# Optimization experiments

Hardware: AMD Instinct MI355X
Metric: run time of the kernel (lower is better)

Reference implementation:

```python
import jax, jax.numpy as jnp
import numpy as np

B, L, D = 1, 512, 768
INIT_STD = 0.02


def setup_inputs() -> dict:
    key = jax.random.key(0)
    ks = jax.random.split(key, 6)
    hidden_states = jax.random.normal(ks[0], (B, L, D), dtype=jnp.float32)
    attention_mask = jnp.zeros((B, 1, L), dtype=jnp.float32)  # additive mask
    # nn.Linear weights, stored as [in, out] so forward is x @ W + b
    Wq = jax.random.normal(ks[1], (D, D), dtype=jnp.float32) * INIT_STD
    bq = jnp.zeros((D,), dtype=jnp.float32)
    Wk = jax.random.normal(ks[2], (D, D), dtype=jnp.float32) * INIT_STD
    bk = jnp.zeros((D,), dtype=jnp.float32)
    w_att = jax.random.normal(ks[3], (D,), dtype=jnp.float32) * INIT_STD  # Linear(D,1)
    b_att = jnp.zeros((), dtype=jnp.float32)
    Wt = jax.random.normal(ks[4], (D, D), dtype=jnp.float32) * INIT_STD
    bt = jnp.zeros((D,), dtype=jnp.float32)
    return {
        "hidden_states": hidden_states,
        "attention_mask": attention_mask,
        "Wq": Wq, "bq": bq, "Wk": Wk, "bk": bk,
        "w_att": w_att, "b_att": b_att, "Wt": Wt, "bt": bt,
    }


def reference(hidden_states, attention_mask, Wq, bq, Wk, bk, w_att, b_att, Wt, bt):
    # Additive (Bahdanau) attention
    Q = hidden_states @ Wq + bq                      # [B, L, D]
    K = hidden_states @ Wk + bk                      # [B, L, D]
    # Broadcast add -> tanh -> linear score: the O(B,L,L,D) intermediate
    feats = jnp.tanh(Q[:, :, None, :] + K[:, None, :, :])   # [B, Lq, Lk, D]
    scores = jnp.einsum('bqkd,d->bqk', feats, w_att) + b_att # [B, Lq, Lk]
    scores = scores + attention_mask                 # additive mask, broadcast
    probs = jax.nn.softmax(scores, axis=-1)          # [B, Lq, Lk]
    weighted = jnp.einsum('bqk,bkd->bqd', probs, hidden_states)  # [B, L, D]
    return weighted @ Wt + bt + Q
```

## Files before the change

kernel.cpp:

```cpp
#include <hip/hip_runtime.h>

#define L 512
#define D 768
#define LL (L * L)
#define LOG2E  1.44269504088896341f
#define LOG2E2 2.88539008177792681f
#define DH 8
#define DSEG (D / DH)
#define QB 8

typedef __attribute__((ext_vector_type(8))) short bf16x8;
typedef __attribute__((ext_vector_type(4))) short bf16x4;
typedef __attribute__((ext_vector_type(4))) float f32x4;
typedef __attribute__((ext_vector_type(2))) float f32x2;

__device__ __forceinline__ ushort f2bf(float f) {
    unsigned u = __builtin_bit_cast(unsigned, f);
    u += 0x7FFFu + ((u >> 16) & 1u);
    return (ushort)(u >> 16);
}

__device__ __forceinline__ unsigned cvt_pk(float lo, float hi) {
    unsigned r;
    asm("v_cvt_pk_bf16_f32 %0, %1, %2" : "=v"(r) : "v"(lo), "v"(hi));
    return r;
}

__device__ __forceinline__ f32x2 dup2(float x) { return (f32x2){x, x}; }

template<int MODE>
__global__ __launch_bounds__(256) void gemm_mfma(
    const float* __restrict__ Xf,
    const float* __restrict__ W0, const float* __restrict__ W1,
    const float* __restrict__ W2,
    const ushort* __restrict__ Abf, const ushort* __restrict__ Btbf,
    const float* __restrict__ bq, const float* __restrict__ bk,
    float* __restrict__ Qb, float* __restrict__ Eq,
    float* __restrict__ EkT, ushort* __restrict__ XWtT,
    const float* __restrict__ bt, const float* __restrict__ addend,
    float* __restrict__ out, int K)
{
    const int N = D;
    const int bz = (MODE == 0) ? blockIdx.z : 0;

    constexpr int BSTR = (MODE == 0) ? 76 : 72;
    __shared__ __align__(16) ushort As[32][72];
    __shared__ __align__(16) ushort Bs[64][BSTR];

    const int m0 = blockIdx.y * 32;
    const int n0 = blockIdx.x * 64;
    const int t = threadIdx.x;
    const int l = t & 63, w = t >> 6;
    const int wr = w >> 1, wc = w & 1;
    const int frow = l & 15;
    const int kg = (l >> 4) * 8;

    f32x4 acc[2] = {};

    auto mfma_step = [&]() {
        bf16x8 af[2], bfr[2][2];
        #pragma unroll
        for (int kk = 0; kk < 2; ++kk) {
            af[kk] = *(const bf16x8*)&As[16 * wr + frow][32 * kk + kg];
            #pragma unroll
            for (int fc = 0; fc < 2; ++fc) {
                if constexpr (MODE == 0) {
                    bf16x4 lo = *(const bf16x4*)&Bs[32 * wc + 16 * fc + frow][32 * kk + kg];
                    bf16x4 hi = *(const bf16x4*)&Bs[32 * wc + 16 * fc + frow][32 * kk + kg + 4];
                    bfr[fc][kk] = __builtin_shufflevector(lo, hi, 0, 1, 2, 3, 4, 5, 6, 7);
                } else {
                    bfr[fc][kk] = *(const bf16x8*)&Bs[32 * wc + 16 * fc + frow][32 * kk + kg];
                }
            }
        }
        #pragma unroll
        for (int fc = 0; fc < 2; ++fc) {
            acc[fc] = __builtin_amdgcn_mfma_f32_16x16x32_bf16(af[0], bfr[fc][0], acc[fc], 0, 0, 0);
            acc[fc] = __builtin_amdgcn_mfma_f32_16x16x32_bf16(af[1], bfr[fc][1], acc[fc], 0, 0, 0);
        }
    };

    if constexpr (MODE == 0) {
        const float* Wm = bz == 0 ? W0 : bz == 1 ? W1 : W2;
        const int srow = t >> 3, sk = (t & 7) * 8;
        const int kq = (t >> 4) * 4, nc = (t & 15) * 4;
        const float* ApF = Xf + (m0 + srow) * D + sk;
        const float* WpF = Wm + kq * D + n0 + nc;

        float4 pa0 = *(const float4*)(ApF + 0);
        float4 pa1 = *(const float4*)(ApF + 4);
        float4 pw0 = *(const float4*)(WpF + 0 * D);
        float4 pw1 = *(const float4*)(WpF + 1 * D);
        float4 pw2 = *(const float4*)(WpF + 2 * D);
        float4 pw3 = *(const float4*)(WpF + 3 * D);

        for (int k0 = 0; k0 < K; k0 += 64) {
            if (k0) __syncthreads();
            {
                uint4 av;
                av.x = cvt_pk(pa0.x, pa0.y);
                av.y = cvt_pk(pa0.z, pa0.w);
                av.z = cvt_pk(pa1.x, pa1.y);
                av.w = cvt_pk(pa1.z, pa1.w);
                *(uint4*)&As[srow][sk] = av;
            }
            {
                uint2 b;
                b.x = cvt_pk(pw0.x, pw1.x); b.y = cvt_pk(pw2.x, pw3.x);
                *(uint2*)&Bs[nc + 0][kq] = b;
                b.x = cvt_pk(pw0.y, pw1.y); b.y = cvt_pk(pw2.y, pw3.y);
                *(uint2*)&Bs[nc + 1][kq] = b;
                b.x = cvt_pk(pw0.z, pw1.z); b.y = cvt_pk(pw2.z, pw3.z);
                *(uint2*)&Bs[nc + 2][kq] = b;
                b.x = cvt_pk(pw0.w, pw1.w); b.y = cvt_pk(pw2.w, pw3.w);
                *(uint2*)&Bs[nc + 3][kq] = b;
            }
            __syncthreads();
            if (k0 + 64 < K) {
                pa0 = *(const float4*)(ApF + k0 + 64);
                pa1 = *(const float4*)(ApF + k0 + 68);
                pw0 = *(const float4*)(WpF + (k0 + 64) * D);
                pw1 = *(const float4*)(WpF + (k0 + 65) * D);
                pw2 = *(const float4*)(WpF + (k0 + 66) * D);
                pw3 = *(const float4*)(WpF + (k0 + 67) * D);
            }
            mfma_step();
        }
    } else {
        const int srow = t >> 3, sk = (t & 7) * 8;
        const ushort* Ap  = Abf  + (m0 + srow) * K + sk;
        const ushort* Bp0 = Btbf + (n0 + srow) * K + sk;
        const ushort* Bp1 = Btbf + (n0 + srow + 32) * K + sk;

        uint4 a0 = *(const uint4*)Ap;
        uint4 b0 = *(const uint4*)Bp0;
        uint4 b1 = *(const uint4*)Bp1;

        for (int k0 = 0; k0 < K; k0 += 64) {
            if (k0) __syncthreads();
            *(uint4*)&As[srow][sk]      = a0;
            *(uint4*)&Bs[srow][sk]      = b0;
            *(uint4*)&Bs[srow + 32][sk] = b1;
            __syncthreads();
            if (k0 + 64 < K) {
                a0 = *(const uint4*)(Ap  + k0 + 64);
                b0 = *(const uint4*)(Bp0 + k0 + 64);
                b1 = *(const uint4*)(Bp1 + k0 + 64);
            }
            mfma_step();
        }
    }

    const int rg = (l >> 4) * 4;
    #pragma unroll
    for (int fc = 0; fc < 2; ++fc) {
        const int col = n0 + 32 * wc + 16 * fc + frow;
        const int row0 = m0 + 16 * wr + rg;
        if (MODE == 0 && bz == 2) {
            uint2 e;
            e.x = cvt_pk(acc[fc][0], acc[fc][1]);
            e.y = cvt_pk(acc[fc][2], acc[fc][3]);
            *(uint2*)&XWtT[col * L + row0] = e;
        } else if (MODE == 0 && bz == 1) {
            const float bv = bk[col];
            float4 e;
            e.x = __builtin_amdgcn_exp2f(LOG2E2 * (acc[fc][0] + bv));
            e.y = __builtin_amdgcn_exp2f(LOG2E2 * (acc[fc][1] + bv));
            e.z = __builtin_amdgcn_exp2f(LOG2E2 * (acc[fc][2] + bv));
            e.w = __builtin_amdgcn_exp2f(LOG2E2 * (acc[fc][3] + bv));
            *(float4*)&EkT[col * L + row0] = e;
        } else if (MODE == 0) {
            const float bv = bq[col];
            #pragma unroll
            for (int i = 0; i < 4; ++i) {
                float v = acc[fc][i] + bv;
                Qb[(row0 + i) * N + col] = v;
                Eq[(row0 + i) * N + col] = __builtin_amdgcn_exp2f(LOG2E2 * v);
            }
        } else {
            const float bv = bt[col];
            #pragma unroll
            for (int i = 0; i < 4; ++i)
                out[(row0 + i) * N + col] =
                    acc[fc][i] + bv + addend[(row0 + i) * N + col];
        }
    }
}

__global__ __launch_bounds__(256) void score_k(
    const float* __restrict__ Eq, const float* __restrict__ EkT,
    const float* __restrict__ w_att, float* __restrict__ sP)
{
    __shared__ __align__(16) float eqlds[DSEG][12];
    const int kt = blockIdx.x;
    const int dh = blockIdx.y;
    const int qg = blockIdx.z;
    const int q0 = qg * QB;
    const int dbase = dh * DSEG;
    const int tid = threadIdx.x;
    const int lane = tid & 63, wv = tid >> 6;
    const int k = kt * 256 + wv * 64 + lane;

    {
        const int row = tid >> 5;
        const int j   = tid & 31;
        #pragma unroll
        for (int c = 0; c < 3; ++c) {
            int d = j + 32 * c;
            eqlds[d][row] = Eq[(q0 + row) * D + dbase + d];
        }
        if (tid < 32) {
            #pragma unroll
            for (int c = 0; c < 3; ++c) {
                int d = tid + 32 * c;
                eqlds[d][8] = (-2.f * LOG2E) * w_att[dbase + d];
            }
        }
    }
    __syncthreads();

    const float* __restrict__ ekp = EkT + dbase * L + k;
    const f32x2 one = dup2(1.f);
    f32x2 acc2[4] = {};

    #pragma unroll 2
    for (int d0 = 0; d0 < DSEG; d0 += 4) {
        f32x2 ek0 = dup2(ekp[(d0 + 0) * L]);
        f32x2 ek1 = dup2(ekp[(d0 + 1) * L]);
        f32x2 ek2 = dup2(ekp[(d0 + 2) * L]);
        f32x2 ek3 = dup2(ekp[(d0 + 3) * L]);
        f32x2 w0 = dup2(eqlds[d0 + 0][8]);
        f32x2 w1 = dup2(eqlds[d0 + 1][8]);
        f32x2 w2 = dup2(eqlds[d0 + 2][8]);
        f32x2 w3 = dup2(eqlds[d0 + 3][8]);
        f32x4 Elo[4], Ehi[4];
        #pragma unroll
        for (int dd = 0; dd < 4; ++dd) {
            Elo[dd] = *(const f32x4*)&eqlds[d0 + dd][0];
            Ehi[dd] = *(const f32x4*)&eqlds[d0 + dd][4];
        }
        #pragma unroll
        for (int j = 0; j < 4; ++j) {
            #define GET2(dd) ((j < 2) ? (f32x2){Elo[dd][2 * j], Elo[dd][2 * j + 1]} \
                                      : (f32x2){Ehi[dd][2 * j - 4], Ehi[dd][2 * j - 3]})
            f32x2 e0 = GET2(0);
            f32x2 e1 = GET2(1);
            f32x2 e2 = GET2(2);
            f32x2 e3 = GET2(3);
            #undef GET2
            f32x2 Aa = __builtin_elementwise_fma(e0, ek0, one);
            f32x2 Bb = __builtin_elementwise_fma(e1, ek1, one);
            f32x2 Cc = __builtin_elementwise_fma(e2, ek2, one);
            f32x2 Dd = __builtin_elementwise_fma(e3, ek3, one);
            f32x2 AB = Aa * Bb, CD = Cc * Dd;
            f32x2 N1 = __builtin_elementwise_fma(w0, Bb, w1 * Aa);
            f32x2 N2 = __builtin_elementwise_fma(w2, Dd, w3 * Cc);
            f32x2 Nm = __builtin_elementwise_fma(N1, CD, N2 * AB);
            f32x2 P = AB * CD;
            f32x2 R;
            R.x = __builtin_amdgcn_rcpf(P.x);
            R.y = __builtin_amdgcn_rcpf(P.y);
            acc2[j] = __builtin_elementwise_fma(Nm, R, acc2[j]);
        }
    }

    float* __restrict__ dst = sP + dh * LL + q0 * L + k;
    #pragma unroll
    for (int j = 0; j < 4; ++j) {
        dst[(2 * j + 0) * L] = acc2[j].x;
        dst[(2 * j + 1) * L] = acc2[j].y;
    }
}

__global__ __launch_bounds__(512) void softmax_probs(
    const float* __restrict__ sP, const float* __restrict__ mask,
    ushort* __restrict__ Pbf)
{
    __shared__ float redB[8];
    const int q = blockIdx.x;
    const int tid = threadIdx.x;
    const int lane = tid & 63, wave = tid >> 6;

    float v = LOG2E * mask[tid];
    #pragma unroll
    for (int h = 0; h < DH; ++h)
        v += sP[h * LL + q * L + tid];

    float e = __builtin_amdgcn_exp2f(v);
    float s = e;
    #pragma unroll
    for (int off = 32; off; off >>= 1)
        s += __shfl_xor(s, off);
    if (lane == 0) redB[wave] = s;
    __syncthreads();
    float t0 = redB[0];
    #pragma unroll
    for (int i = 1; i < 8; ++i) t0 += redB[i];
    Pbf[q * L + tid] = f2bf(e * __builtin_amdgcn_rcpf(t0));
}

extern "C" void kernel_launch(void* const* d_in, const int* in_sizes, int n_in,
                              void* d_out, int out_size, void* d_ws, size_t ws_size,
                              hipStream_t stream) {
    const float* X     = (const float*)d_in[0];
    const float* mask  = (const float*)d_in[1];
    const float* Wq    = (const float*)d_in[2];
    const float* bq    = (const float*)d_in[3];
    const float* Wk    = (const float*)d_in[4];
    const float* bk    = (const float*)d_in[5];
    const float* w_att = (const float*)d_in[6];
    const float* Wt    = (const float*)d_in[8];
    const float* bt    = (const float*)d_in[9];
    float* out = (float*)d_out;

    const int LD = L * D;
    float*  Qb   = (float*)d_ws;
    float*  Eq   = Qb + LD;
    float*  EkT  = Eq + LD;
    float*  sP   = EkT + LD;
    ushort* XWtT = (ushort*)(sP + DH * LL);
    ushort* Pbf  = XWtT + LD;

    gemm_mfma<0><<<dim3(D / 64, L / 32, 3), 256, 0, stream>>>(
        X, Wq, Wk, Wt, nullptr, nullptr, bq, bk,
        Qb, Eq, EkT, XWtT, nullptr, nullptr, nullptr, D);

    score_k<<<dim3(2, DH, L / QB), 256, 0, stream>>>(Eq, EkT, w_att, sP);

    softmax_probs<<<dim3(L), 512, 0, stream>>>(sP, mask, Pbf);

    gemm_mfma<1><<<dim3(D / 64, L / 32, 1), 256, 0, stream>>>(
        nullptr, nullptr, nullptr, nullptr, Pbf, XWtT, nullptr, nullptr,
        nullptr, nullptr, nullptr, nullptr, bt, Qb, out, L);
}
```

Baseline: 45.78 us.

## Fuse three projection GEMMs to share X tile, widen PV GEMM to 8 waves

The first GEMM now computes the Q, K and Wt projections in one block that loads and converts each X tile once and keeps three accumulator sets, instead of a z-dimension of three separate blocks. This cuts redundant X loads and bf16 conversions but gives a third as many blocks (192) with more registers and LDS per block. The PV GEMM becomes a dedicated 512-thread kernel with 8 waves, each holding one 16x16 tile, to raise per-block parallelism. The score kernel moves the attention weights into their own LDS array so they can be read with one vector load.

```diff
diff --git a/kernel.cpp b/kernel.cpp
--- a/kernel.cpp
+++ b/kernel.cpp
@@ -28,24 +28,17 @@
 
 __device__ __forceinline__ f32x2 dup2(float x) { return (f32x2){x, x}; }
 
-template<int MODE>
-__global__ __launch_bounds__(256) void gemm_mfma(
+__global__ __launch_bounds__(256) void gemm_fused0(
     const float* __restrict__ Xf,
     const float* __restrict__ W0, const float* __restrict__ W1,
     const float* __restrict__ W2,
-    const ushort* __restrict__ Abf, const ushort* __restrict__ Btbf,
     const float* __restrict__ bq, const float* __restrict__ bk,
     float* __restrict__ Qb, float* __restrict__ Eq,
-    float* __restrict__ EkT, ushort* __restrict__ XWtT,
-    const float* __restrict__ bt, const float* __restrict__ addend,
-    float* __restrict__ out, int K)
+    float* __restrict__ EkT, ushort* __restrict__ XWtT)
 {
-    const int N = D;
-    const int bz = (MODE == 0) ? blockIdx.z : 0;
-
-    constexpr int BSTR = (MODE == 0) ? 76 : 72;
+    const int N = D, K = D;
     __shared__ __align__(16) ushort As[32][72];
-    __shared__ __align__(16) ushort Bs[64][BSTR];
+    __shared__ __align__(16) ushort Bs[3][64][76];
 
     const int m0 = blockIdx.y * 32;
     const int n0 = blockIdx.x * 64;
@@ -55,100 +48,74 @@
     const int frow = l & 15;
     const int kg = (l >> 4) * 8;
 
-    f32x4 acc[2] = {};
-
-    auto mfma_step = [&]() {
-        bf16x8 af[2], bfr[2][2];
-        #pragma unroll
-        for (int kk = 0; kk < 2; ++kk) {
+    const int srow = t >> 3, sk = (t & 7) * 8;
+    const int kq = (t >> 4) * 4, nc = (t & 15) * 4;
+    const float* ApF = Xf + (m0 + srow) * D + sk;
+    const float* Wp0 = W0 + kq * D + n0 + nc;
+    const float* Wp1 = W1 + kq * D + n0 + nc;
+    const float* Wp2 = W2 + kq * D + n0 + nc;
+
+    float4 pa0 = *(const float4*)(ApF + 0);
+    float4 pa1 = *(const float4*)(ApF + 4);
+    float4 pw[3][4];
+    #pragma unroll
+    for (int r = 0; r < 4; ++r) {
+        pw[0][r] = *(const float4*)(Wp0 + r * D);
+        pw[1][r] = *(const float4*)(Wp1 + r * D);
+        pw[2][r] = *(const float4*)(Wp2 + r * D);
+    }
+
+    f32x4 acc[3][2] = {};
+
+    for (int k0 = 0; k0 < K; k0 += 64) {
+        if (k0) __syncthreads();
+        {
+            uint4 av;
+            av.x = cvt_pk(pa0.x, pa0.y);
+            av.y = cvt_pk(pa0.z, pa0.w);
+            av.z = cvt_pk(pa1.x, pa1.y);
+            av.w = cvt_pk(pa1.z, pa1.w);
+            *(uint4*)&As[srow][sk] = av;
+        }
+        #pragma unroll
+        for (int m = 0; m < 3; ++m) {
+            uint2 b;
+            b.x = cvt_pk(pw[m][0].x, pw[m][1].x); b.y = cvt_pk(pw[m][2].x, pw[m][3].x);
+            *(uint2*)&Bs[m][nc + 0][kq] = b;
+            b.x = cvt_pk(pw[m][0].y, pw[m][1].y); b.y = cvt_pk(pw[m][2].y, pw[m][3].y);
+            *(uint2*)&Bs[m][nc + 1][kq] = b;
+            b.x = cvt_pk(pw[m][0].z, pw[m][1].z); b.y = cvt_pk(pw[m][2].z, pw[m][3].z);
+            *(uint2*)&Bs[m][nc + 2][kq] = b;
+            b.x = cvt_pk(pw[m][0].w, pw[m][1].w); b.y = cvt_pk(pw[m][2].w, pw[m][3].w);
+            *(uint2*)&Bs[m][nc + 3][kq] = b;
+        }
+        __syncthreads();
+        if (k0 + 64 < K) {
+            pa0 = *(const float4*)(ApF + k0 + 64);
+            pa1 = *(const float4*)(ApF + k0 + 68);
+            #pragma unroll
+            for (int r = 0; r < 4; ++r) {
+                pw[0][r] = *(const float4*)(Wp0 + (k0 + 64 + r) * D);
+                pw[1][r] = *(const float4*)(Wp1 + (k0 + 64 + r) * D);
+                pw[2][r] = *(const float4*)(Wp2 + (k0 + 64 + r) * D);
+            }
+        }
+
+        bf16x8 af[2];
+        #pragma unroll
+        for (int kk = 0; kk < 2; ++kk)
             af[kk] = *(const bf16x8*)&As[16 * wr + frow][32 * kk + kg];
+        #pragma unroll
+        for (int m = 0; m < 3; ++m)
             #pragma unroll
-            for (int fc = 0; fc < 2; ++fc) {
-                if constexpr (MODE == 0) {
-                    bf16x4 lo = *(const bf16x4*)&Bs[32 * wc + 16 * fc + frow][32 * kk + kg];
-                    bf16x4 hi = *(const bf16x4*)&Bs[32 * wc + 16 * fc + frow][32 * kk + kg + 4];
-                    bfr[fc][kk] = __builtin_shufflevector(lo, hi, 0, 1, 2, 3, 4, 5, 6, 7);
-                } else {
-                    bfr[fc][kk] = *(const bf16x8*)&Bs[32 * wc + 16 * fc + frow][32 * kk + kg];
+            for (int fc = 0; fc < 2; ++fc)
+                #pragma unroll
+                for (int kk = 0; kk < 2; ++kk) {
+                    bf16x4 lo = *(const bf16x4*)&Bs[m][32 * wc + 16 * fc + frow][32 * kk + kg];
+                    bf16x4 hi = *(const bf16x4*)&Bs[m][32 * wc + 16 * fc + frow][32 * kk + kg + 4];
+                    bf16x8 bv = __builtin_shufflevector(lo, hi, 0, 1, 2, 3, 4, 5, 6, 7);
+                    acc[m][fc] = __builtin_amdgcn_mfma_f32_16x16x32_bf16(af[kk], bv, acc[m][fc], 0, 0, 0);
                 }
-            }
-        }
-        #pragma unroll
-        for (int fc = 0; fc < 2; ++fc) {
-            acc[fc] = __builtin_amdgcn_mfma_f32_16x16x32_bf16(af[0], bfr[fc][0], acc[fc], 0, 0, 0);
-            acc[fc] = __builtin_amdgcn_mfma_f32_16x16x32_bf16(af[1], bfr[fc][1], acc[fc], 0, 0, 0);
-        }
-    };
-
-    if constexpr (MODE == 0) {
-        const float* Wm = bz == 0 ? W0 : bz == 1 ? W1 : W2;
-        const int srow = t >> 3, sk = (t & 7) * 8;
-        const int kq = (t >> 4) * 4, nc = (t & 15) * 4;
-        const float* ApF = Xf + (m0 + srow) * D + sk;
-        const float* WpF = Wm + kq * D + n0 + nc;
-
-        float4 pa0 = *(const float4*)(ApF + 0);
-        float4 pa1 = *(const float4*)(ApF + 4);
-        float4 pw0 = *(const float4*)(WpF + 0 * D);
-        float4 pw1 = *(const float4*)(WpF + 1 * D);
-        float4 pw2 = *(const float4*)(WpF + 2 * D);
-        float4 pw3 = *(const float4*)(WpF + 3 * D);
-
-        for (int k0 = 0; k0 < K; k0 += 64) {
-            if (k0) __syncthreads();
-            {
-                uint4 av;
-                av.x = cvt_pk(pa0.x, pa0.y);
-                av.y = cvt_pk(pa0.z, pa0.w);
-                av.z = cvt_pk(pa1.x, pa1.y);
-                av.w = cvt_pk(pa1.z, pa1.w);
-                *(uint4*)&As[srow][sk] = av;
-            }
-            {
-                uint2 b;
-                b.x = cvt_pk(pw0.x, pw1.x); b.y = cvt_pk(pw2.x, pw3.x);
-                *(uint2*)&Bs[nc + 0][kq] = b;
-                b.x = cvt_pk(pw0.y, pw1.y); b.y = cvt_pk(pw2.y, pw3.y);
-                *(uint2*)&Bs[nc + 1][kq] = b;
-                b.x = cvt_pk(pw0.z, pw1.z); b.y = cvt_pk(pw2.z, pw3.z);
-                *(uint2*)&Bs[nc + 2][kq] = b;
-                b.x = cvt_pk(pw0.w, pw1.w); b.y = cvt_pk(pw2.w, pw3.w);
-                *(uint2*)&Bs[nc + 3][kq] = b;
-            }
-            __syncthreads();
-            if (k0 + 64 < K) {
-                pa0 = *(const float4*)(ApF + k0 + 64);
-                pa1 = *(const float4*)(ApF + k0 + 68);
-                pw0 = *(const float4*)(WpF + (k0 + 64) * D);
-                pw1 = *(const float4*)(WpF + (k0 + 65) * D);
-                pw2 = *(const float4*)(WpF + (k0 + 66) * D);
-                pw3 = *(const float4*)(WpF + (k0 + 67) * D);
-            }
-            mfma_step();
-        }
-    } else {
-        const int srow = t >> 3, sk = (t & 7) * 8;
-        const ushort* Ap  = Abf  + (m0 + srow) * K + sk;
-        const ushort* Bp0 = Btbf + (n0 + srow) * K + sk;
-        const ushort* Bp1 = Btbf + (n0 + srow + 32) * K + sk;
-
-        uint4 a0 = *(const uint4*)Ap;
-        uint4 b0 = *(const uint4*)Bp0;
-        uint4 b1 = *(const uint4*)Bp1;
-
-        for (int k0 = 0; k0 < K; k0 += 64) {
-            if (k0) __syncthreads();
-            *(uint4*)&As[srow][sk]      = a0;
-            *(uint4*)&Bs[srow][sk]      = b0;
-            *(uint4*)&Bs[srow + 32][sk] = b1;
-            __syncthreads();
-            if (k0 + 64 < K) {
-                a0 = *(const uint4*)(Ap  + k0 + 64);
-                b0 = *(const uint4*)(Bp0 + k0 + 64);
-                b1 = *(const uint4*)(Bp1 + k0 + 64);
-            }
-            mfma_step();
-        }
     }
 
     const int rg = (l >> 4) * 4;
@@ -156,42 +123,92 @@
     for (int fc = 0; fc < 2; ++fc) {
         const int col = n0 + 32 * wc + 16 * fc + frow;
         const int row0 = m0 + 16 * wr + rg;
-        if (MODE == 0 && bz == 2) {
-            uint2 e;
-            e.x = cvt_pk(acc[fc][0], acc[fc][1]);
-            e.y = cvt_pk(acc[fc][2], acc[fc][3]);
-            *(uint2*)&XWtT[col * L + row0] = e;
-        } else if (MODE == 0 && bz == 1) {
-            const float bv = bk[col];
-            float4 e;
-            e.x = __builtin_amdgcn_exp2f(LOG2E2 * (acc[fc][0] + bv));
-            e.y = __builtin_amdgcn_exp2f(LOG2E2 * (acc[fc][1] + bv));
-            e.z = __builtin_amdgcn_exp2f(LOG2E2 * (acc[fc][2] + bv));
-            e.w = __builtin_amdgcn_exp2f(LOG2E2 * (acc[fc][3] + bv));
-            *(float4*)&EkT[col * L + row0] = e;
-        } else if (MODE == 0) {
+        {
             const float bv = bq[col];
             #pragma unroll
             for (int i = 0; i < 4; ++i) {
-                float v = acc[fc][i] + bv;
+                float v = acc[0][fc][i] + bv;
                 Qb[(row0 + i) * N + col] = v;
                 Eq[(row0 + i) * N + col] = __builtin_amdgcn_exp2f(LOG2E2 * v);
             }
-        } else {
-            const float bv = bt[col];
-            #pragma unroll
-            for (int i = 0; i < 4; ++i)
-                out[(row0 + i) * N + col] =
-                    acc[fc][i] + bv + addend[(row0 + i) * N + col];
-        }
-    }
+        }
+        {
+            const float bv = bk[col];
+            float4 e;
+            e.x = __builtin_amdgcn_exp2f(LOG2E2 * (acc[1][fc][0] + bv));
+            e.y = __builtin_amdgcn_exp2f(LOG2E2 * (acc[1][fc][1] + bv));
+            e.z = __builtin_amdgcn_exp2f(LOG2E2 * (acc[1][fc][2] + bv));
+            e.w = __builtin_amdgcn_exp2f(LOG2E2 * (acc[1][fc][3] + bv));
+            *(float4*)&EkT[col * L + row0] = e;
+        }
+        {
+            uint2 e;
+            e.x = cvt_pk(acc[2][fc][0], acc[2][fc][1]);
+            e.y = cvt_pk(acc[2][fc][2], acc[2][fc][3]);
+            *(uint2*)&XWtT[col * L + row0] = e;
+        }
+    }
+}
+
+__global__ __launch_bounds__(512) void gemm_pv(
+    const ushort* __restrict__ Pbf, const ushort* __restrict__ XWtT,
+    const float* __restrict__ bt, const float* __restrict__ Qb,
+    float* __restrict__ out)
+{
+    const int N = D, K = L;
+    __shared__ __align__(16) ushort As[32][72];
+    __shared__ __align__(16) ushort Bs[64][72];
+
+    const int m0 = blockIdx.y * 32;
+    const int n0 = blockIdx.x * 64;
+    const int t = threadIdx.x;
+    const int l = t & 63, w = t >> 6;
+    const int wr = w >> 2, wc = w & 3;
+    const int frow = l & 15;
+    const int kg = (l >> 4) * 8;
+
+    const int srA = t >> 4, skA = (t & 15) * 4;
+    const int srB = t >> 3, skB = (t & 7) * 8;
+    const ushort* Ap = Pbf  + (m0 + srA) * K + skA;
+    const ushort* Bp = XWtT + (n0 + srB) * K + skB;
+
+    uint2 a0 = *(const uint2*)Ap;
+    uint4 b0 = *(const uint4*)Bp;
+
+    f32x4 acc = {};
+
+    for (int k0 = 0; k0 < K; k0 += 64) {
+        if (k0) __syncthreads();
+        *(uint2*)&As[srA][skA] = a0;
+        *(uint4*)&Bs[srB][skB] = b0;
+        __syncthreads();
+        if (k0 + 64 < K) {
+            a0 = *(const uint2*)(Ap + k0 + 64);
+            b0 = *(const uint4*)(Bp + k0 + 64);
+        }
+        #pragma unroll
+        for (int kk = 0; kk < 2; ++kk) {
+            bf16x8 af = *(const bf16x8*)&As[16 * wr + frow][32 * kk + kg];
+            bf16x8 bv = *(const bf16x8*)&Bs[16 * wc + frow][32 * kk + kg];
+            acc = __builtin_amdgcn_mfma_f32_16x16x32_bf16(af, bv, acc, 0, 0, 0);
+        }
+    }
+
+    const int rg = (l >> 4) * 4;
+    const int col = n0 + 16 * wc + frow;
+    const int row0 = m0 + 16 * wr + rg;
+    const float bv = bt[col];
+    #pragma unroll
+    for (int i = 0; i < 4; ++i)
+        out[(row0 + i) * N + col] = acc[i] + bv + Qb[(row0 + i) * N + col];
 }
 
 __global__ __launch_bounds__(256) void score_k(
     const float* __restrict__ Eq, const float* __restrict__ EkT,
     const float* __restrict__ w_att, float* __restrict__ sP)
 {
-    __shared__ __align__(16) float eqlds[DSEG][12];
+    __shared__ __align__(16) float eqlds[DSEG][8];
+    __shared__ __align__(16) float wlds[DSEG];
     const int kt = blockIdx.x;
     const int dh = blockIdx.y;
     const int qg = blockIdx.z;
@@ -213,7 +230,7 @@
             #pragma unroll
             for (int c = 0; c < 3; ++c) {
                 int d = tid + 32 * c;
-                eqlds[d][8] = (-2.f * LOG2E) * w_att[dbase + d];
+                wlds[d] = (-2.f * LOG2E) * w_att[dbase + d];
             }
         }
     }
@@ -229,10 +246,9 @@
         f32x2 ek1 = dup2(ekp[(d0 + 1) * L]);
         f32x2 ek2 = dup2(ekp[(d0 + 2) * L]);
         f32x2 ek3 = dup2(ekp[(d0 + 3) * L]);
-        f32x2 w0 = dup2(eqlds[d0 + 0][8]);
-        f32x2 w1 = dup2(eqlds[d0 + 1][8]);
-        f32x2 w2 = dup2(eqlds[d0 + 2][8]);
-        f32x2 w3 = dup2(eqlds[d0 + 3][8]);
+        f32x4 wq4 = *(const f32x4*)&wlds[d0];
+        f32x2 w0 = dup2(wq4[0]), w1 = dup2(wq4[1]);
+        f32x2 w2 = dup2(wq4[2]), w3 = dup2(wq4[3]);
         f32x4 Elo[4], Ehi[4];
         #pragma unroll
         for (int dd = 0; dd < 4; ++dd) {
@@ -321,15 +337,12 @@
     ushort* XWtT = (ushort*)(sP + DH * LL);
     ushort* Pbf  = XWtT + LD;
 
-    gemm_mfma<0><<<dim3(D / 64, L / 32, 3), 256, 0, stream>>>(
-        X, Wq, Wk, Wt, nullptr, nullptr, bq, bk,
-        Qb, Eq, EkT, XWtT, nullptr, nullptr, nullptr, D);
+    gemm_fused0<<<dim3(D / 64, L / 32), 256, 0, stream>>>(
+        X, Wq, Wk, Wt, bq, bk, Qb, Eq, EkT, XWtT);
 
     score_k<<<dim3(2, DH, L / QB), 256, 0, stream>>>(Eq, EkT, w_att, sP);
 
     softmax_probs<<<dim3(L), 512, 0, stream>>>(sP, mask, Pbf);
 
-    gemm_mfma<1><<<dim3(D / 64, L / 32, 1), 256, 0, stream>>>(
-        nullptr, nullptr, nullptr, nullptr, Pbf, XWtT, nullptr, nullptr,
-        nullptr, nullptr, nullptr, nullptr, bt, Qb, out, L);
-}
+    gemm_pv<<<dim3(D / 64, L / 32), 512, 0, stream>>>(Pbf, XWtT, bt, Qb, out);
+}
```

New measurement: 49.61 us. 1.08x slower.
